# Performance work log

Hardware: AMD Instinct MI355X
Metric: run time of the kernel (lower is better)

Reference implementation:

```python
import jax, jax.numpy as jnp
import numpy as np
from jax import lax

N = 8192          # number of proposals
CLASSES = 81      # includes background class 0
PAD = 300         # padding (max detections kept)
NMS_THRESH = 0.5


def _decode_and_pick(metadata, deltas, proposals, scores):
    """bbox_transform_inv + clip + per-row argmax class gather (keras_rcnn math)."""
    scale = metadata[0, 2]
    boxes = proposals.reshape(-1, 4) / scale                      # (N,4) x1,y1,x2,y2
    n = boxes.shape[0]
    d = deltas.reshape(n, -1, 4)                                  # (N,C,4) dx,dy,dw,dh
    s = scores.reshape(n, -1)                                     # (N,C)

    w = boxes[:, 2] - boxes[:, 0] + 1.0
    h = boxes[:, 3] - boxes[:, 1] + 1.0
    cx = boxes[:, 0] + 0.5 * w
    cy = boxes[:, 1] + 0.5 * h

    pcx = d[:, :, 0] * w[:, None] + cx[:, None]
    pcy = d[:, :, 1] * h[:, None] + cy[:, None]
    pw = jnp.exp(d[:, :, 2]) * w[:, None]
    ph = jnp.exp(d[:, :, 3]) * h[:, None]

    pred = jnp.stack([pcx - 0.5 * pw, pcy - 0.5 * ph,
                      pcx + 0.5 * pw, pcy + 0.5 * ph], axis=-1)   # (N,C,4)

    # clip to image: x cols to [0, W-1], y cols to [0, H-1]; metadata[0,:2]=(H,W)
    H, W = metadata[0, 0], metadata[0, 1]
    lim = jnp.stack([W - 1.0, H - 1.0, W - 1.0, H - 1.0])
    pred = jnp.clip(pred, 0.0, lim)

    top = jnp.argmax(s, axis=1)                                   # (N,)
    sel = jnp.take_along_axis(pred, top[:, None, None], axis=1)[:, 0, :]  # (N,4)
    max_scores = jnp.max(s[:, 1:], axis=1)                        # exclude background
    return sel, s, max_scores


def _nms_indices(boxes, scores):
    """Greedy NMS; returns (PAD,) kept indices + float validity mask."""
    n = boxes.shape[0]
    order = jnp.argsort(-scores)
    b = boxes[order]
    x1, y1, x2, y2 = b[:, 0], b[:, 1], b[:, 2], b[:, 3]
    area = jnp.maximum(x2 - x1, 0.0) * jnp.maximum(y2 - y1, 0.0)
    lt = jnp.maximum(b[:, None, :2], b[None, :, :2])
    rb = jnp.minimum(b[:, None, 2:], b[None, :, 2:])
    wh = jnp.maximum(rb - lt, 0.0)
    inter = wh[..., 0] * wh[..., 1]                               # (N,N)
    iou = inter / (area[:, None] + area[None, :] - inter + 1e-8)

    idx = jnp.arange(n)

    def step(suppressed, xs):
        iou_row, i = xs
        keep_i = jnp.logical_not(suppressed[i])
        suppressed = suppressed | (keep_i & (iou_row > NMS_THRESH) & (idx > i))
        return suppressed, keep_i

    _, keep = lax.scan(step, jnp.zeros((n,), bool), (iou, idx))    # keep in sorted order

    rank = jnp.cumsum(keep.astype(jnp.int32)) - 1
    pos = jnp.where(keep & (rank < PAD), rank, PAD)               # overflow slot PAD
    buf = jnp.zeros((PAD + 1,), jnp.int32).at[pos].set(order.astype(jnp.int32))
    keep_idx = buf[:PAD]
    num_kept = jnp.minimum(jnp.sum(keep.astype(jnp.int32)), PAD)
    valid = (jnp.arange(PAD) < num_kept).astype(boxes.dtype)
    return keep_idx, valid


def setup_inputs() -> dict:
    key = jax.random.key(0)
    k1, k2, k3, k4, k5, k6 = jax.random.split(key, 6)
    Himg, Wimg, scale = 800.0, 1333.0, 1.5
    metadata = jnp.array([[Himg, Wimg, scale]], dtype=jnp.float32)
    cx = jax.random.uniform(k1, (1, N), minval=0.0, maxval=Wimg * scale)
    cy = jax.random.uniform(k2, (1, N), minval=0.0, maxval=Himg * scale)
    w = jax.random.uniform(k3, (1, N), minval=16.0, maxval=256.0)
    h = jax.random.uniform(k4, (1, N), minval=16.0, maxval=256.0)
    proposals = jnp.stack([cx - 0.5 * w, cy - 0.5 * h,
                           cx + 0.5 * w, cy + 0.5 * h], axis=-1)  # (1,N,4)
    deltas = 0.1 * jax.random.normal(k5, (1, N, 4 * CLASSES), dtype=jnp.float32)
    scores = jax.random.uniform(k6, (1, N, CLASSES), dtype=jnp.float32)
    return {"metadata": metadata, "deltas": deltas,
            "proposals": proposals, "scores": scores}


def reference(metadata, deltas, proposals, scores):
    sel, s, max_scores = _decode_and_pick(metadata, deltas, proposals, scores)
    keep_idx, valid = _nms_indices(lax.stop_gradient(sel),
                                   lax.stop_gradient(max_scores))
    boxes_out = sel[keep_idx] * valid[:, None]                    # (PAD,4), zero-padded
    scores_out = s[keep_idx] * valid[:, None]                     # (PAD,C)
    return boxes_out[None], scores_out[None]
```

## Files before the change

kernel.cpp:

```cpp
#include <hip/hip_runtime.h>

#define N 8192
#define NCLS 81
#define PAD 300
#define NPANEL 16
#define PANW 512

typedef unsigned long long u64;

__device__ __forceinline__ void gload_lds16(const void* g, void* l) {
  __builtin_amdgcn_global_load_lds(
      (const __attribute__((address_space(1))) unsigned int*)g,
      (__attribute__((address_space(3))) unsigned int*)l, 16, 0, 0);
}

__global__ __launch_bounds__(256) void decode_kernel(
    const float* __restrict__ meta, const float* __restrict__ deltas,
    const float* __restrict__ proposals, const float* __restrict__ scores,
    float4* __restrict__ sel, u64* __restrict__ keys, int* __restrict__ rank,
    int* __restrict__ ctr) {
  int tid = threadIdx.x;
  if (blockIdx.x == 0 && tid < 16) ctr[tid] = 0;
  int row = blockIdx.x * 32 + (tid >> 3);
  int sub = tid & 7;
  const float* srow = scores + (size_t)row * NCLS;
  float bs = -1e30f, ms = -1e30f;
  int best = 0;
  for (int c = sub; c < NCLS; c += 8) {
    float v = srow[c];
    if (v > bs) { bs = v; best = c; }
    if (c > 0) ms = fmaxf(ms, v);
  }
#pragma unroll
  for (int d = 1; d < 8; d <<= 1) {
    float ob = __shfl_xor(bs, d);
    int oi = __shfl_xor(best, d);
    float om = __shfl_xor(ms, d);
    if (ob > bs || (ob == bs && oi < best)) { bs = ob; best = oi; }
    ms = fmaxf(ms, om);
  }
  if (sub == 0) {
    float W = meta[1], sc = meta[2], H = meta[0];
    const float* p = proposals + row * 4;
    float x1 = p[0] / sc, y1 = p[1] / sc, x2 = p[2] / sc, y2 = p[3] / sc;
    float w = x2 - x1 + 1.0f, h = y2 - y1 + 1.0f;
    float cx = x1 + 0.5f * w, cy = y1 + 0.5f * h;
    float4 d4 = *(const float4*)(deltas + (size_t)row * (4 * NCLS) + best * 4);
    float pcx = d4.x * w + cx, pcy = d4.y * h + cy;
    float pw = expf(d4.z) * w, ph = expf(d4.w) * h;
    float lx = W - 1.0f, ly = H - 1.0f;
    float ox1 = fminf(fmaxf(pcx - 0.5f * pw, 0.0f), lx);
    float oy1 = fminf(fmaxf(pcy - 0.5f * ph, 0.0f), ly);
    float ox2 = fminf(fmaxf(pcx + 0.5f * pw, 0.0f), lx);
    float oy2 = fminf(fmaxf(pcy + 0.5f * ph, 0.0f), ly);
    sel[row] = make_float4(ox1, oy1, ox2, oy2);
    keys[row] = ((u64)(~__float_as_uint(ms)) << 32) | (unsigned)row;
    rank[row] = 0;
  }
}

__global__ __launch_bounds__(256) void rank_kernel(
    const u64* __restrict__ keys, int* __restrict__ rank) {
  __shared__ u64 kt[256];
  int tid = threadIdx.x;
  int i = blockIdx.x * 256 + tid;
  kt[tid] = keys[blockIdx.y * 256 + tid];
  u64 ki = keys[i];
  __syncthreads();
  int c = 0;
#pragma unroll 8
  for (int t = 0; t < 256; ++t) c += (kt[t] < ki);
  atomicAdd(&rank[i], c);
}

__global__ __launch_bounds__(256) void scatter_kernel(
    const int* __restrict__ rank, const float4* __restrict__ sel,
    int* __restrict__ sortedIdx, float4* __restrict__ sortedBoxes,
    float* __restrict__ sortedArea) {
  int i = blockIdx.x * 256 + threadIdx.x;
  int r = rank[i];
  float4 b = sel[i];
  sortedIdx[r] = i;
  sortedBoxes[r] = b;
  sortedArea[r] = fmaxf(b.z - b.x, 0.0f) * fmaxf(b.w - b.y, 0.0f);
}

__global__ __launch_bounds__(256) void mask_scan_kernel(
    const float4* __restrict__ sboxes, const float* __restrict__ sarea,
    u64* __restrict__ mask, int* __restrict__ kept, int* __restrict__ num_kept,
    int* __restrict__ ctr) {
  __shared__ union {
    u64 slab[PANW * 8];
    struct { float4 cbox[256]; float carea[256]; } m;
  } sh;
  __shared__ int keptGi[PAD];
  int tid = threadIdx.x;

  if (blockIdx.x > 0) {
    int idx = (int)blockIdx.x - 1;
    int cb = idx >> 5, rg = idx & 31;
    if (4 * rg > cb) return;
    int rbase = rg * 256;
    sh.m.cbox[tid] = sboxes[rbase + tid];
    sh.m.carea[tid] = sarea[rbase + tid];
    int lane = tid & 63, wid = tid >> 6;
    float4 bj = sboxes[cb * 64 + lane];
    float aB = sarea[cb * 64 + lane];
    __syncthreads();
    int rlim = cb * 64 + 64;
    int r0 = rbase + (wid << 6);
#pragma unroll 4
    for (int i = 0; i < 32; ++i) {
      int r1 = r0 + i, r2 = r0 + i + 32;
      if (r1 >= rlim) break;
      float4 bi1 = sh.m.cbox[(wid << 6) + i];
      float aA1 = sh.m.carea[(wid << 6) + i];
      float4 bi2 = sh.m.cbox[(wid << 6) + i + 32];
      float aA2 = sh.m.carea[(wid << 6) + i + 32];
      float lx1 = fmaxf(bi1.x, bj.x), ly1 = fmaxf(bi1.y, bj.y);
      float rx1 = fminf(bi1.z, bj.z), ry1 = fminf(bi1.w, bj.w);
      float in1 = fmaxf(rx1 - lx1, 0.0f) * fmaxf(ry1 - ly1, 0.0f);
      float u1 = aA1 + aB - in1 + 1e-8f;
      u64 bits1 = __ballot(((in1 * 33554432.0f - u1 * 16777216.0f) - u1) > 0.0f);
      float lx2 = fmaxf(bi2.x, bj.x), ly2 = fmaxf(bi2.y, bj.y);
      float rx2 = fminf(bi2.z, bj.z), ry2 = fminf(bi2.w, bj.w);
      float in2 = fmaxf(rx2 - lx2, 0.0f) * fmaxf(ry2 - ly2, 0.0f);
      float u2 = aA2 + aB - in2 + 1e-8f;
      u64 bits2 = __ballot(((in2 * 33554432.0f - u2 * 16777216.0f) - u2) > 0.0f);
      if ((r1 >> 6) == cb) bits1 &= ~((2ull << (r1 & 63)) - 1ull);
      if ((r2 >> 6) == cb) bits2 &= ~((2ull << (r2 & 63)) - 1ull);
      if (lane == 0) {
        __hip_atomic_store(&mask[(size_t)r1 * 128 + cb], bits1,
                           __ATOMIC_RELAXED, __HIP_MEMORY_SCOPE_AGENT);
        if (r2 < rlim)
          __hip_atomic_store(&mask[(size_t)r2 * 128 + cb], bits2,
                             __ATOMIC_RELAXED, __HIP_MEMORY_SCOPE_AGENT);
      }
    }
    __syncthreads();
    if (tid == 0)
      __hip_atomic_fetch_add(&ctr[cb >> 3], 1, __ATOMIC_RELEASE,
                             __HIP_MEMORY_SCOPE_AGENT);
    return;
  }

  if (tid >= 64) return;
  int lane = tid;
  int cnt = 0;
  const char* mb = (const char*)mask;

  for (int p = 0; p < NPANEL; ++p) {
    int base = p * PANW;
    int need = 16 * p + 12;
    while (__hip_atomic_load(&ctr[p], __ATOMIC_RELAXED,
                             __HIP_MEMORY_SCOPE_AGENT) < need)
      __builtin_amdgcn_s_sleep(8);
    (void)__hip_atomic_load(&ctr[p], __ATOMIC_ACQUIRE,
                            __HIP_MEMORY_SCOPE_AGENT);

    {
      const char* srcB = mb + (size_t)base * 1024 + (size_t)p * 64;
#pragma unroll
      for (int it = 0; it < 16; ++it) {
        const char* g = srcB + (size_t)(it * 16 + (lane >> 2)) * 1024 + (lane & 3) * 16;
        gload_lds16(g, &sh.slab[0] + it * 128);
      }
    }
    u64 acc = 0ull;
    for (int k = (lane >> 3); k < cnt; k += 8)
      acc |= mask[(size_t)keptGi[k] * 128 + p * 8 + (lane & 7)];

    asm volatile("s_waitcnt vmcnt(0)" ::: "memory");
    __builtin_amdgcn_sched_barrier(0);

    {
      const char* srcB = mb + (size_t)(base + 256) * 1024 + (size_t)p * 64;
#pragma unroll
      for (int it = 0; it < 16; ++it) {
        const char* g = srcB + (size_t)(it * 16 + (lane >> 2)) * 1024 + (lane & 3) * 16;
        gload_lds16(g, &sh.slab[0] + (16 + it) * 128);
      }
    }

    acc |= __shfl_xor(acc, 8);
    acc |= __shfl_xor(acc, 16);
    acc |= __shfl_xor(acc, 32);
    u64 remv = acc;
    const u64* sl = sh.slab;
    bool h2 = false;

    unsigned wm = (unsigned)__ballot(~remv != 0ull) & 0xFFu;
    while (cnt < PAD && wm) {
      int w = __ffs(wm) - 1;
      if (w >= 4 && !h2) {
        asm volatile("s_waitcnt vmcnt(0)" ::: "memory");
        __builtin_amdgcn_sched_barrier(0);
        h2 = true;
      }
      u64 cur = __shfl(remv, w);
      u64 inv = ~cur;
      int b1 = __ffsll(inv) - 1;
      u64 i2 = inv & (inv - 1);
      int b2 = i2 ? (__ffsll(i2) - 1) : -1;
      u64 i3 = i2 ? (i2 & (i2 - 1)) : 0ull;
      int b3 = i3 ? (__ffsll(i3) - 1) : -1;
      u64 i4 = i3 ? (i3 & (i3 - 1)) : 0ull;
      int b4 = i4 ? (__ffsll(i4) - 1) : -1;
      int li1 = (w << 6) + b1;
      int li2 = (b2 >= 0) ? ((w << 6) + b2) : li1;
      int li3 = (b3 >= 0) ? ((w << 6) + b3) : li1;
      int li4 = (b4 >= 0) ? ((w << 6) + b4) : li1;
      u64 mA1 = sl[li1 * 8 + w], sA1 = sl[li1 * 8 + (lane & 7)];
      u64 mA2 = sl[li2 * 8 + w], sA2 = sl[li2 * 8 + (lane & 7)];
      u64 mA3 = sl[li3 * 8 + w], sA3 = sl[li3 * 8 + (lane & 7)];
      u64 mA4 = sl[li4 * 8 + w], sA4 = sl[li4 * 8 + (lane & 7)];
      bool k2 = (b2 >= 0) && !((mA1 >> b2) & 1ull);
      bool k3 = (b3 >= 0) && !((mA1 >> b3) & 1ull) && !(k2 && ((mA2 >> b3) & 1ull));
      bool k4 = (b4 >= 0) && !((mA1 >> b4) & 1ull) && !(k2 && ((mA2 >> b4) & 1ull)) &&
                !(k3 && ((mA3 >> b4) & 1ull));
      u64 ownbits = 1ull << b1;
      if (lane == 0) kept[cnt] = base + li1;
      keptGi[cnt] = base + li1;
      cnt++;
      remv |= sA1;
      if (cnt < PAD && k2) {
        if (lane == 0) kept[cnt] = base + li2;
        keptGi[cnt] = base + li2;
        cnt++;
        remv |= sA2;
        ownbits |= 1ull << b2;
      }
      if (cnt < PAD && k3) {
        if (lane == 0) kept[cnt] = base + li3;
        keptGi[cnt] = base + li3;
        cnt++;
        remv |= sA3;
        ownbits |= 1ull << b3;
      }
      if (cnt < PAD && k4) {
        if (lane == 0) kept[cnt] = base + li4;
        keptGi[cnt] = base + li4;
        cnt++;
        remv |= sA4;
        ownbits |= 1ull << b4;
      }
      if ((lane & 7) == w) remv |= ownbits;
      wm = (unsigned)__ballot(~remv != 0ull) & 0xFFu;
    }
    if (cnt >= PAD) break;
  }
  asm volatile("s_waitcnt vmcnt(0)" ::: "memory");
  if (lane == 0) *num_kept = cnt;
}

__global__ __launch_bounds__(128) void gather_kernel(
    const int* __restrict__ kept, const int* __restrict__ num_kept_p,
    const int* __restrict__ sortedIdx, const float4* __restrict__ sortedBoxes,
    const float* __restrict__ scores, float* __restrict__ out) {
  int r = blockIdx.x;
  int t = threadIdx.x;
  float* boxes_out = out;
  float* scores_out = out + PAD * 4;
  int nk = *num_kept_p;
  bool valid = r < nk;
  int pos = valid ? kept[r] : 0;
  if (t < NCLS) {
    int orig = sortedIdx[pos];
    scores_out[(size_t)r * NCLS + t] = valid ? scores[(size_t)orig * NCLS + t] : 0.0f;
  }
  if (t == 96) {
    float4 b = sortedBoxes[pos];
    if (!valid) b = make_float4(0.f, 0.f, 0.f, 0.f);
    ((float4*)boxes_out)[r] = b;
  }
}

extern "C" void kernel_launch(void* const* d_in, const int* in_sizes, int n_in,
                              void* d_out, int out_size, void* d_ws, size_t ws_size,
                              hipStream_t stream) {
  const float* meta = (const float*)d_in[0];
  const float* deltas = (const float*)d_in[1];
  const float* proposals = (const float*)d_in[2];
  const float* scores = (const float*)d_in[3];
  float* out = (float*)d_out;
  char* ws = (char*)d_ws;

  float4* sel = (float4*)(ws + 0);
  u64* keys = (u64*)(ws + 131072);
  int* rank = (int*)(ws + 196608);
  int* sortedIdx = (int*)(ws + 229376);
  float4* sortedBoxes = (float4*)(ws + 262144);
  float* sortedArea = (float*)(ws + 393216);
  int* kept = (int*)(ws + 425984);
  int* num_kept = (int*)(ws + 428032);
  int* ctr = (int*)(ws + 428096);
  u64* mask = (u64*)(ws + 458752);

  decode_kernel<<<N / 32, 256, 0, stream>>>(meta, deltas, proposals, scores, sel, keys, rank, ctr);
  rank_kernel<<<dim3(N / 256, N / 256), 256, 0, stream>>>(keys, rank);
  scatter_kernel<<<N / 256, 256, 0, stream>>>(rank, sel, sortedIdx, sortedBoxes, sortedArea);
  mask_scan_kernel<<<1 + 128 * 32, 256, 0, stream>>>(sortedBoxes, sortedArea, mask, kept, num_kept, ctr);
  gather_kernel<<<PAD, 128, 0, stream>>>(kept, num_kept, sortedIdx, sortedBoxes, scores, out);
}
```

Baseline: 88.57 us.

## Resolve intra-word NMS chain via register diagonal blocks and readlane

```diff
diff --git a/kernel.cpp b/kernel.cpp
--- a/kernel.cpp
+++ b/kernel.cpp
@@ -12,6 +12,12 @@
   __builtin_amdgcn_global_load_lds(
       (const __attribute__((address_space(1))) unsigned int*)g,
       (__attribute__((address_space(3))) unsigned int*)l, 16, 0, 0);
+}
+
+__device__ __forceinline__ u64 readlane64(u64 v, int l) {
+  unsigned lo = __builtin_amdgcn_readlane((unsigned)v, l);
+  unsigned hi = __builtin_amdgcn_readlane((unsigned)(v >> 32), l);
+  return ((u64)hi << 32) | lo;
 }
 
 __global__ __launch_bounds__(256) void decode_kernel(
@@ -161,90 +167,59 @@
     {
       const char* srcB = mb + (size_t)base * 1024 + (size_t)p * 64;
 #pragma unroll
-      for (int it = 0; it < 16; ++it) {
+      for (int it = 0; it < 32; ++it) {
         const char* g = srcB + (size_t)(it * 16 + (lane >> 2)) * 1024 + (lane & 3) * 16;
         gload_lds16(g, &sh.slab[0] + it * 128);
       }
     }
+    u64 d0 = mask[(size_t)(base + 0 + lane) * 128 + p * 8 + 0];
+    u64 d1 = mask[(size_t)(base + 64 + lane) * 128 + p * 8 + 1];
+    u64 d2 = mask[(size_t)(base + 128 + lane) * 128 + p * 8 + 2];
+    u64 d3 = mask[(size_t)(base + 192 + lane) * 128 + p * 8 + 3];
+    u64 d4 = mask[(size_t)(base + 256 + lane) * 128 + p * 8 + 4];
+    u64 d5 = mask[(size_t)(base + 320 + lane) * 128 + p * 8 + 5];
+    u64 d6 = mask[(size_t)(base + 384 + lane) * 128 + p * 8 + 6];
+    u64 d7 = mask[(size_t)(base + 448 + lane) * 128 + p * 8 + 7];
     u64 acc = 0ull;
     for (int k = (lane >> 3); k < cnt; k += 8)
       acc |= mask[(size_t)keptGi[k] * 128 + p * 8 + (lane & 7)];
 
     asm volatile("s_waitcnt vmcnt(0)" ::: "memory");
     __builtin_amdgcn_sched_barrier(0);
-
-    {
-      const char* srcB = mb + (size_t)(base + 256) * 1024 + (size_t)p * 64;
-#pragma unroll
-      for (int it = 0; it < 16; ++it) {
-        const char* g = srcB + (size_t)(it * 16 + (lane >> 2)) * 1024 + (lane & 3) * 16;
-        gload_lds16(g, &sh.slab[0] + (16 + it) * 128);
-      }
-    }
 
     acc |= __shfl_xor(acc, 8);
     acc |= __shfl_xor(acc, 16);
     acc |= __shfl_xor(acc, 32);
     u64 remv = acc;
     const u64* sl = sh.slab;
-    bool h2 = false;
 
     unsigned wm = (unsigned)__ballot(~remv != 0ull) & 0xFFu;
     while (cnt < PAD && wm) {
       int w = __ffs(wm) - 1;
-      if (w >= 4 && !h2) {
-        asm volatile("s_waitcnt vmcnt(0)" ::: "memory");
-        __builtin_amdgcn_sched_barrier(0);
-        h2 = true;
-      }
+      u64 diagW = (w == 0) ? d0 : (w == 1) ? d1 : (w == 2) ? d2 : (w == 3) ? d3
+                : (w == 4) ? d4 : (w == 5) ? d5 : (w == 6) ? d6 : d7;
       u64 cur = __shfl(remv, w);
-      u64 inv = ~cur;
-      int b1 = __ffsll(inv) - 1;
-      u64 i2 = inv & (inv - 1);
-      int b2 = i2 ? (__ffsll(i2) - 1) : -1;
-      u64 i3 = i2 ? (i2 & (i2 - 1)) : 0ull;
-      int b3 = i3 ? (__ffsll(i3) - 1) : -1;
-      u64 i4 = i3 ? (i3 & (i3 - 1)) : 0ull;
-      int b4 = i4 ? (__ffsll(i4) - 1) : -1;
-      int li1 = (w << 6) + b1;
-      int li2 = (b2 >= 0) ? ((w << 6) + b2) : li1;
-      int li3 = (b3 >= 0) ? ((w << 6) + b3) : li1;
-      int li4 = (b4 >= 0) ? ((w << 6) + b4) : li1;
-      u64 mA1 = sl[li1 * 8 + w], sA1 = sl[li1 * 8 + (lane & 7)];
-      u64 mA2 = sl[li2 * 8 + w], sA2 = sl[li2 * 8 + (lane & 7)];
-      u64 mA3 = sl[li3 * 8 + w], sA3 = sl[li3 * 8 + (lane & 7)];
-      u64 mA4 = sl[li4 * 8 + w], sA4 = sl[li4 * 8 + (lane & 7)];
-      bool k2 = (b2 >= 0) && !((mA1 >> b2) & 1ull);
-      bool k3 = (b3 >= 0) && !((mA1 >> b3) & 1ull) && !(k2 && ((mA2 >> b3) & 1ull));
-      bool k4 = (b4 >= 0) && !((mA1 >> b4) & 1ull) && !(k2 && ((mA2 >> b4) & 1ull)) &&
-                !(k3 && ((mA3 >> b4) & 1ull));
-      u64 ownbits = 1ull << b1;
-      if (lane == 0) kept[cnt] = base + li1;
-      keptGi[cnt] = base + li1;
-      cnt++;
-      remv |= sA1;
-      if (cnt < PAD && k2) {
-        if (lane == 0) kept[cnt] = base + li2;
-        keptGi[cnt] = base + li2;
+      u64 kb = 0ull;
+      while (true) {
+        u64 inv = ~cur;
+        if (inv == 0ull) break;
+        int b = __ffsll(inv) - 1;
+        u64 mrow = readlane64(diagW, b);
+        if (lane == 0) kept[cnt] = base + (w << 6) + b;
+        keptGi[cnt] = base + (w << 6) + b;
         cnt++;
-        remv |= sA2;
-        ownbits |= 1ull << b2;
-      }
-      if (cnt < PAD && k3) {
-        if (lane == 0) kept[cnt] = base + li3;
-        keptGi[cnt] = base + li3;
-        cnt++;
-        remv |= sA3;
-        ownbits |= 1ull << b3;
-      }
-      if (cnt < PAD && k4) {
-        if (lane == 0) kept[cnt] = base + li4;
-        keptGi[cnt] = base + li4;
-        cnt++;
-        remv |= sA4;
-        ownbits |= 1ull << b4;
-      }
-      if ((lane & 7) == w) remv |= ownbits;
+        kb |= 1ull << b;
+        cur |= mrow | (1ull << b);
+        if (cnt >= PAD) break;
+      }
+      u64 t = kb;
+      while (t) {
+        int b = __ffsll(t) - 1;
+        t &= t - 1;
+        remv |= sl[((w << 6) + b) * 8 + (lane & 7)];
+      }
+      if ((lane & 7) == w) remv |= kb;
+      if (cnt >= PAD) break;
       wm = (unsigned)__ballot(~remv != 0ull) & 0xFFu;
     }
     if (cnt >= PAD) break;
```

New measurement: 88.70 us. Within noise of the previous version (+0.1%).

## Fuse rank and scatter via last-block counter; load full mask panel upfront

Applied to the files above, without the earlier changes.

```diff
diff --git a/kernel.cpp b/kernel.cpp
--- a/kernel.cpp
+++ b/kernel.cpp
@@ -20,7 +20,7 @@
     float4* __restrict__ sel, u64* __restrict__ keys, int* __restrict__ rank,
     int* __restrict__ ctr) {
   int tid = threadIdx.x;
-  if (blockIdx.x == 0 && tid < 16) ctr[tid] = 0;
+  if (blockIdx.x == 0 && tid < 48) ctr[tid] = 0;
   int row = blockIdx.x * 32 + (tid >> 3);
   int sub = tid & 7;
   const float* srow = scores + (size_t)row * NCLS;
@@ -59,11 +59,16 @@
   }
 }
 
-__global__ __launch_bounds__(256) void rank_kernel(
-    const u64* __restrict__ keys, int* __restrict__ rank) {
+__global__ __launch_bounds__(256) void rank_scatter_kernel(
+    const u64* __restrict__ keys, int* __restrict__ rank,
+    const float4* __restrict__ sel, int* __restrict__ sortedIdx,
+    float4* __restrict__ sortedBoxes, float* __restrict__ sortedArea,
+    int* __restrict__ rctr) {
   __shared__ u64 kt[256];
+  __shared__ int lastFlag;
   int tid = threadIdx.x;
-  int i = blockIdx.x * 256 + tid;
+  int bx = blockIdx.x;
+  int i = bx * 256 + tid;
   kt[tid] = keys[blockIdx.y * 256 + tid];
   u64 ki = keys[i];
   __syncthreads();
@@ -71,18 +76,20 @@
 #pragma unroll 8
   for (int t = 0; t < 256; ++t) c += (kt[t] < ki);
   atomicAdd(&rank[i], c);
-}
-
-__global__ __launch_bounds__(256) void scatter_kernel(
-    const int* __restrict__ rank, const float4* __restrict__ sel,
-    int* __restrict__ sortedIdx, float4* __restrict__ sortedBoxes,
-    float* __restrict__ sortedArea) {
-  int i = blockIdx.x * 256 + threadIdx.x;
-  int r = rank[i];
-  float4 b = sel[i];
-  sortedIdx[r] = i;
-  sortedBoxes[r] = b;
-  sortedArea[r] = fmaxf(b.z - b.x, 0.0f) * fmaxf(b.w - b.y, 0.0f);
+  __syncthreads();
+  if (tid == 0) {
+    int prev = __hip_atomic_fetch_add(&rctr[bx], 1, __ATOMIC_ACQ_REL,
+                                      __HIP_MEMORY_SCOPE_AGENT);
+    lastFlag = (prev == 31);
+  }
+  __syncthreads();
+  if (lastFlag) {
+    int r = __hip_atomic_load(&rank[i], __ATOMIC_RELAXED, __HIP_MEMORY_SCOPE_AGENT);
+    float4 b = sel[i];
+    sortedIdx[r] = i;
+    sortedBoxes[r] = b;
+    sortedArea[r] = fmaxf(b.z - b.x, 0.0f) * fmaxf(b.w - b.y, 0.0f);
+  }
 }
 
 __global__ __launch_bounds__(256) void mask_scan_kernel(
@@ -161,7 +168,7 @@
     {
       const char* srcB = mb + (size_t)base * 1024 + (size_t)p * 64;
 #pragma unroll
-      for (int it = 0; it < 16; ++it) {
+      for (int it = 0; it < 32; ++it) {
         const char* g = srcB + (size_t)(it * 16 + (lane >> 2)) * 1024 + (lane & 3) * 16;
         gload_lds16(g, &sh.slab[0] + it * 128);
       }
@@ -172,31 +179,16 @@
 
     asm volatile("s_waitcnt vmcnt(0)" ::: "memory");
     __builtin_amdgcn_sched_barrier(0);
-
-    {
-      const char* srcB = mb + (size_t)(base + 256) * 1024 + (size_t)p * 64;
-#pragma unroll
-      for (int it = 0; it < 16; ++it) {
-        const char* g = srcB + (size_t)(it * 16 + (lane >> 2)) * 1024 + (lane & 3) * 16;
-        gload_lds16(g, &sh.slab[0] + (16 + it) * 128);
-      }
-    }
 
     acc |= __shfl_xor(acc, 8);
     acc |= __shfl_xor(acc, 16);
     acc |= __shfl_xor(acc, 32);
     u64 remv = acc;
     const u64* sl = sh.slab;
-    bool h2 = false;
 
     unsigned wm = (unsigned)__ballot(~remv != 0ull) & 0xFFu;
     while (cnt < PAD && wm) {
       int w = __ffs(wm) - 1;
-      if (w >= 4 && !h2) {
-        asm volatile("s_waitcnt vmcnt(0)" ::: "memory");
-        __builtin_amdgcn_sched_barrier(0);
-        h2 = true;
-      }
       u64 cur = __shfl(remv, w);
       u64 inv = ~cur;
       int b1 = __ffsll(inv) - 1;
@@ -297,8 +289,8 @@
   u64* mask = (u64*)(ws + 458752);
 
   decode_kernel<<<N / 32, 256, 0, stream>>>(meta, deltas, proposals, scores, sel, keys, rank, ctr);
-  rank_kernel<<<dim3(N / 256, N / 256), 256, 0, stream>>>(keys, rank);
-  scatter_kernel<<<N / 256, 256, 0, stream>>>(rank, sel, sortedIdx, sortedBoxes, sortedArea);
+  rank_scatter_kernel<<<dim3(N / 256, N / 256), 256, 0, stream>>>(
+      keys, rank, sel, sortedIdx, sortedBoxes, sortedArea, ctr + 16);
   mask_scan_kernel<<<1 + 128 * 32, 256, 0, stream>>>(sortedBoxes, sortedArea, mask, kept, num_kept, ctr);
   gather_kernel<<<PAD, 128, 0, stream>>>(kept, num_kept, sortedIdx, sortedBoxes, scores, out);
 }
```

Result: slower. 94.06 us (+6.2%).
